# Optimization experiments

Measured on AMD Instinct MI355X. Metric: run time of the kernel, lower is better.

## Reference

```python
import jax, jax.numpy as jnp
import numpy as np

N_NODES = 131072
N_EDGES = 1048576
N_FEAT = 8
H = 128
H6 = 256
N_PROB = 64


def _gru_cell(m, h, Wih, Whh, bih, bhh):
    # PyTorch GRUCell semantics
    gi = m @ Wih.T + bih  # [N, 3H]
    gh = h @ Whh.T + bhh
    i_r, i_z, i_n = jnp.split(gi, 3, axis=-1)
    h_r, h_z, h_n = jnp.split(gh, 3, axis=-1)
    r = jax.nn.sigmoid(i_r + h_r)
    z = jax.nn.sigmoid(i_z + h_z)
    n = jnp.tanh(i_n + r * h_n)
    return (1.0 - z) * n + z * h


def _gated_graph_conv(x, src, dst, ew, W, Wih, Whh, bih, bhh):
    # PyG GatedGraphConv(out_channels=H, num_layers=2); in_channels == out_channels so no padding
    h = x
    for l in range(2):
        t = h @ W[l]                      # node-level transform [N, H]
        msg = t[src] * ew[:, None]        # gather + edge scaling [E, H]
        agg = jax.ops.segment_sum(msg, dst, num_segments=x.shape[0])  # scatter-add
        h = _gru_cell(agg, h, Wih, Whh, bih, bhh)
    return h


def _forward(G, edge_index, edge_weight, edge_attribute, segment_ids,
             W_emb1, b_emb1, W_emb2, b_emb2,
             conv1_W, conv1_Wih, conv1_Whh, conv1_bih, conv1_bhh,
             conv2_W, conv2_Wih, conv2_Whh, conv2_bih, conv2_bhh,
             W_g1, b_g1, W_g2, b_g2, W_l, b_l, W_l2, b_l2, W_l3, b_l3):
    src, dst = edge_index[0], edge_index[1]
    x = jax.nn.relu(G @ W_emb1 + b_emb1)
    x = jax.nn.relu(x @ W_emb2 + b_emb2)
    x = jax.nn.relu(_gated_graph_conv(x, src, dst, edge_weight, conv1_W, conv1_Wih, conv1_Whh, conv1_bih, conv1_bhh))
    x = jax.nn.relu(_gated_graph_conv(x, src, dst, edge_weight, conv2_W, conv2_Wih, conv2_Whh, conv2_bih, conv2_bhh))
    x = jax.nn.relu(x @ W_g1 + b_g1)
    x = x @ W_g2 + b_g2                   # node embeddings [N, H]
    # per-problem segment mean (replaces the python loop over contiguous slices)
    sums = jax.ops.segment_sum(x, segment_ids, num_segments=N_PROB)
    counts = jax.ops.segment_sum(jnp.ones((x.shape[0], 1), x.dtype), segment_ids, num_segments=N_PROB)
    gmean = sums / jnp.maximum(counts, 1.0)
    u = jnp.concatenate([x, gmean[segment_ids]], axis=-1)  # [N, 2H]
    u = jax.nn.relu(u @ W_l + b_l)
    u = jax.nn.relu(u @ W_l2 + b_l2)
    u = u @ W_l3 + b_l3                   # [N, 1]
    return u


def setup_inputs() -> dict:
    key = jax.random.key(0)
    ks = jax.random.split(key, 40)
    s = 0.05
    rn = lambda k, shp: (jax.random.normal(k, shp, jnp.float32) * s)
    inp = {}
    inp["G"] = jax.random.normal(ks[0], (N_NODES, N_FEAT), jnp.float32)
    inp["edge_index"] = jax.random.randint(ks[1], (2, N_EDGES), 0, N_NODES, jnp.int32)
    inp["edge_weight"] = jax.random.uniform(ks[2], (N_EDGES,), jnp.float32)
    inp["edge_attribute"] = jax.random.normal(ks[3], (N_EDGES,), jnp.float32)
    inp["segment_ids"] = jnp.sort(jax.random.randint(ks[4], (N_NODES,), 0, N_PROB, jnp.int32))
    inp["W_emb1"] = rn(ks[5], (N_FEAT, H)); inp["b_emb1"] = jnp.zeros((H,), jnp.float32)
    inp["W_emb2"] = rn(ks[6], (H, H));      inp["b_emb2"] = jnp.zeros((H,), jnp.float32)
    inp["conv1_W"] = rn(ks[7], (2, H, H))
    inp["conv1_Wih"] = rn(ks[8], (3 * H, H)); inp["conv1_Whh"] = rn(ks[9], (3 * H, H))
    inp["conv1_bih"] = jnp.zeros((3 * H,), jnp.float32); inp["conv1_bhh"] = jnp.zeros((3 * H,), jnp.float32)
    inp["conv2_W"] = rn(ks[10], (2, H, H))
    inp["conv2_Wih"] = rn(ks[11], (3 * H, H)); inp["conv2_Whh"] = rn(ks[12], (3 * H, H))
    inp["conv2_bih"] = jnp.zeros((3 * H,), jnp.float32); inp["conv2_bhh"] = jnp.zeros((3 * H,), jnp.float32)
    inp["W_g1"] = rn(ks[13], (H, H)); inp["b_g1"] = jnp.zeros((H,), jnp.float32)
    inp["W_g2"] = rn(ks[14], (H, H)); inp["b_g2"] = jnp.zeros((H,), jnp.float32)
    inp["W_l"] = rn(ks[15], (2 * H, H6)); inp["b_l"] = jnp.zeros((H6,), jnp.float32)
    inp["W_l2"] = rn(ks[16], (H6, H)); inp["b_l2"] = jnp.zeros((H,), jnp.float32)
    inp["W_l3"] = rn(ks[17], (H, 1)); inp["b_l3"] = jnp.zeros((1,), jnp.float32)
    return inp


def reference(G, edge_index, edge_weight, edge_attribute, segment_ids,
              W_emb1, b_emb1, W_emb2, b_emb2,
              conv1_W, conv1_Wih, conv1_Whh, conv1_bih, conv1_bhh,
              conv2_W, conv2_Wih, conv2_Whh, conv2_bih, conv2_bhh,
              W_g1, b_g1, W_g2, b_g2, W_l, b_l, W_l2, b_l2, W_l3, b_l3):
    return _forward(G, edge_index, edge_weight, edge_attribute, segment_ids,
                    W_emb1, b_emb1, W_emb2, b_emb2,
                    conv1_W, conv1_Wih, conv1_Whh, conv1_bih, conv1_bhh,
                    conv2_W, conv2_Wih, conv2_Whh, conv2_bih, conv2_bhh,
                    W_g1, b_g1, W_g2, b_g2, W_l, b_l, W_l2, b_l2, W_l3, b_l3)
```

## Files before the change

kernel.cpp:

```cpp
#include <hip/hip_runtime.h>
#include <cstdint>
#include <cstddef>

#define NNODES 131072
#define NEDGES 1048576
#define NPROB  64

typedef _Float16 half8 __attribute__((ext_vector_type(8)));
typedef _Float16 half4v __attribute__((ext_vector_type(4)));
typedef _Float16 half2v __attribute__((ext_vector_type(2)));
typedef float float4v __attribute__((ext_vector_type(4)));

__device__ __forceinline__ float fsigm(float x) {
    return __builtin_amdgcn_rcpf(1.0f + __expf(-x));
}
__device__ __forceinline__ float ftanh(float x) {
    return 1.0f - 2.0f * __builtin_amdgcn_rcpf(__expf(2.0f * x) + 1.0f);
}

__device__ __forceinline__ void async16(void* lds, const void* g) {
    __builtin_amdgcn_global_load_lds(
        (const __attribute__((address_space(1))) uint32_t*)g,
        (__attribute__((address_space(3))) uint32_t*)lds, 16, 0, 0);
}

__global__ __launch_bounds__(256) void cvt16(const float* __restrict__ s,
                                             _Float16* __restrict__ d, int n)
{
    int i = blockIdx.x * 256 + threadIdx.x;
    if (i < n) d[i] = (_Float16)s[i];
}

__global__ __launch_bounds__(256) void tr_cvt(const float* __restrict__ src,
    _Float16* __restrict__ dst, int K, int M, int sstride)
{
    int i = blockIdx.x * 256 + threadIdx.x;
    if (i < M * K) {
        int m = i / K, k = i % K;
        dst[i] = (_Float16)src[(size_t)k * sstride + m];
    }
}

__global__ __launch_bounds__(256) void deg_hist(const int* __restrict__ dst,
                                                int* __restrict__ deg)
{
    int e = blockIdx.x * 256 + threadIdx.x;
    atomicAdd(&deg[dst[e]], 1);
}

__global__ __launch_bounds__(256) void scan1(const int* __restrict__ deg,
    int* __restrict__ offs, int* __restrict__ bsum)
{
    __shared__ int s[256];
    int b = blockIdx.x, tid = threadIdx.x;
    int4 v = ((const int4*)deg)[b * 256 + tid];
    int t0 = v.x, t1 = t0 + v.y, t2 = t1 + v.z, t3 = t2 + v.w;
    s[tid] = t3;
    __syncthreads();
    for (int off = 1; off < 256; off <<= 1) {
        int x = (tid >= off) ? s[tid - off] : 0;
        __syncthreads();
        if (tid >= off) s[tid] += x;
        __syncthreads();
    }
    int excl = tid ? s[tid - 1] : 0;
    int4 o; o.x = excl; o.y = excl + t0; o.z = excl + t1; o.w = excl + t2;
    ((int4*)offs)[b * 256 + tid] = o;
    if (tid == 255) bsum[b] = s[255];
}

__global__ __launch_bounds__(128) void scan2(int* __restrict__ bsum)
{
    __shared__ int s[128];
    int tid = threadIdx.x;
    s[tid] = bsum[tid];
    __syncthreads();
    for (int off = 1; off < 128; off <<= 1) {
        int x = (tid >= off) ? s[tid - off] : 0;
        __syncthreads();
        if (tid >= off) s[tid] += x;
        __syncthreads();
    }
    bsum[tid] = tid ? s[tid - 1] : 0;
}

__global__ __launch_bounds__(256) void scan3(int* __restrict__ offs,
    const int* __restrict__ bsum, int* __restrict__ pos)
{
    int i = blockIdx.x * 256 + threadIdx.x;
    int v = offs[i] + bsum[i >> 10];
    offs[i] = v;
    pos[i] = v;
    if (i == 0) offs[NNODES] = NEDGES;
}

__global__ __launch_bounds__(256) void csr_fill(const int* __restrict__ src,
    const int* __restrict__ dst, const float* __restrict__ ew,
    int* __restrict__ pos, int2* __restrict__ csr)
{
    int e = blockIdx.x * 256 + threadIdx.x;
    int slot = atomicAdd(&pos[dst[e]], 1);
    csr[slot] = make_int2(src[e], __float_as_int(ew[e]));
}

__global__ __launch_bounds__(256) void gather_agg(const _Float16* __restrict__ t,
    const int2* __restrict__ csr, const int* __restrict__ offs,
    _Float16* __restrict__ agg)
{
    int node = blockIdx.x * 4 + (threadIdx.x >> 6);
    int lane = threadIdx.x & 63;
    int i = offs[node], end = offs[node + 1];
    float a0 = 0.0f, a1 = 0.0f;
    int2 p;
    if (i < end) p = csr[i];
    while (i < end) {
        int2 cur = p;
        if (i + 1 < end) p = csr[i + 1];
        float w = __int_as_float(cur.y);
        half2v v = *(const half2v*)(t + (size_t)cur.x * 128 + lane * 2);
        a0 = fmaf((float)v[0], w, a0);
        a1 = fmaf((float)v[1], w, a1);
        ++i;
    }
    half2v o; o[0] = (_Float16)a0; o[1] = (_Float16)a1;
    *(half2v*)(agg + (size_t)node * 128 + lane * 2) = o;
}

__global__ __launch_bounds__(256) void emb1_kernel(const float* __restrict__ G,
    const float* __restrict__ W1, const float* __restrict__ b1, _Float16* __restrict__ Y)
{
    int idx = blockIdx.x * 256 + threadIdx.x;
    int n = idx >> 7, c = idx & 127;
    const float* g = G + (size_t)n * 8;
    float y = b1[c];
#pragma unroll
    for (int k = 0; k < 8; ++k) y = fmaf(g[k], W1[k * 128 + c], y);
    Y[(size_t)n * 128 + c] = (_Float16)fmaxf(y, 0.0f);
}

template<int K, int MCH, bool INF16, bool RELU, bool SEGADD>
__global__ __launch_bounds__(256, 2) void gemm_mfma(
    const void* __restrict__ Xin, int xstride,
    const _Float16* __restrict__ Wt,
    const float* __restrict__ bias,
    _Float16* __restrict__ out1, int ostride,
    const float* __restrict__ gproj, const int* __restrict__ seg)
{
    constexpr int ROWB = 2 * K;
    constexpr int SPR  = K / 8;
    __shared__ __align__(16) char Xs[128 * ROWB];
    __shared__ __align__(16) char Ws[128 * ROWB];
    const int tid = threadIdx.x, wid = tid >> 6, l = tid & 63;
    const int lr = l & 15, lk = l >> 4;
    const int wrow = wid * 32;

    for (int mc = 0; mc < MCH; ++mc) {
        __syncthreads();
        {
            const _Float16* wsrc = Wt + (size_t)mc * 128 * K;
            for (int s0 = wid * 64; s0 < 128 * SPR; s0 += 256) {
                int s = s0 + l;
                int row = s / SPR, sub = s % SPR;
                int ksub = sub ^ (row & 7);
                async16(Ws + s0 * 16, (const char*)(wsrc + (size_t)row * K) + ksub * 16);
            }
        }
        asm volatile("s_waitcnt vmcnt(0)" ::: "memory");
        __syncthreads();

        half8 bfr[32];
        if constexpr (K == 128) {
#pragma unroll
            for (int ct = 0; ct < 8; ++ct)
#pragma unroll
                for (int ks = 0; ks < 4; ++ks) {
                    int row = ct * 16 + lr;
                    bfr[ct * 4 + ks] = *(const half8*)(Ws + row * ROWB +
                        ((ks * 64 + lk * 16) ^ ((row & 7) << 4)));
                }
        }

        for (int t = blockIdx.x; t < NNODES / 128; t += gridDim.x) {
            const int nbase = t * 128;
            __syncthreads();
            if constexpr (INF16) {
                const _Float16* xsrc = (const _Float16*)Xin;
                for (int s0 = wid * 64; s0 < 128 * SPR; s0 += 256) {
                    int s = s0 + l;
                    int row = s / SPR, sub = s % SPR;
                    int ksub = sub ^ (row & 7);
                    async16(Xs + s0 * 16,
                            (const char*)(xsrc + (size_t)(nbase + row) * xstride) + ksub * 16);
                }
                asm volatile("s_waitcnt vmcnt(0)" ::: "memory");
            } else {
                const float* xsrc = (const float*)Xin;
                for (int s = tid; s < 128 * SPR; s += 256) {
                    int row = s / SPR, sub = s % SPR;
                    int ksub = sub ^ (row & 7);
                    const float* p = xsrc + (size_t)(nbase + row) * xstride + ksub * 8;
                    float4 u = ((const float4*)p)[0];
                    float4 v = ((const float4*)p)[1];
                    half8 hv;
                    hv[0] = (_Float16)u.x; hv[1] = (_Float16)u.y;
                    hv[2] = (_Float16)u.z; hv[3] = (_Float16)u.w;
                    hv[4] = (_Float16)v.x; hv[5] = (_Float16)v.y;
                    hv[6] = (_Float16)v.z; hv[7] = (_Float16)v.w;
                    *(half8*)(Xs + s * 16) = hv;
                }
            }
            __syncthreads();

            float4v acc[2][8];
#pragma unroll
            for (int i = 0; i < 2; ++i)
#pragma unroll
                for (int j = 0; j < 8; ++j)
#pragma unroll
                    for (int q = 0; q < 4; ++q) acc[i][j][q] = 0.0f;

            if constexpr (K == 128) {
#pragma unroll
                for (int rt = 0; rt < 2; ++rt) {
                    half8 a[4];
                    int row = wrow + rt * 16 + lr;
#pragma unroll
                    for (int ks = 0; ks < 4; ++ks)
                        a[ks] = *(const half8*)(Xs + row * ROWB +
                            ((ks * 64 + lk * 16) ^ ((row & 7) << 4)));
#pragma unroll
                    for (int ct = 0; ct < 8; ++ct)
#pragma unroll
                        for (int ks = 0; ks < 4; ++ks)
                            acc[rt][ct] = __builtin_amdgcn_mfma_f32_16x16x32_f16(
                                a[ks], bfr[ct * 4 + ks], acc[rt][ct], 0, 0, 0);
                }
            } else {
#pragma unroll
                for (int kc = 0; kc < 2; ++kc) {
#pragma unroll
                    for (int ct = 0; ct < 8; ++ct)
#pragma unroll
                        for (int ks = 0; ks < 4; ++ks) {
                            int row = ct * 16 + lr;
                            bfr[ct * 4 + ks] = *(const half8*)(Ws + row * ROWB +
                                (((kc * 4 + ks) * 64 + lk * 16) ^ ((row & 7) << 4)));
                        }
#pragma unroll
                    for (int rt = 0; rt < 2; ++rt) {
                        half8 a[4];
                        int row = wrow + rt * 16 + lr;
#pragma unroll
                        for (int ks = 0; ks < 4; ++ks)
                            a[ks] = *(const half8*)(Xs + row * ROWB +
                                (((kc * 4 + ks) * 64 + lk * 16) ^ ((row & 7) << 4)));
#pragma unroll
                        for (int ct = 0; ct < 8; ++ct)
#pragma unroll
                            for (int ks = 0; ks < 4; ++ks)
                                acc[rt][ct] = __builtin_amdgcn_mfma_f32_16x16x32_f16(
                                    a[ks], bfr[ct * 4 + ks], acc[rt][ct], 0, 0, 0);
                    }
                }
            }

#pragma unroll
            for (int rt = 0; rt < 2; ++rt)
#pragma unroll
            for (int ct = 0; ct < 8; ++ct) {
                const int col = ct * 16 + lr;
                float bv = 0.0f;
                if (bias) bv = bias[mc * 128 + col];
#pragma unroll
                for (int j = 0; j < 4; ++j) {
                    const int n = nbase + wrow + rt * 16 + lk * 4 + j;
                    float v = acc[rt][ct][j] + bv;
                    if constexpr (SEGADD)
                        v += gproj[(size_t)seg[n] * 256 + mc * 128 + col];
                    if constexpr (RELU) v = fmaxf(v, 0.0f);
                    out1[(size_t)n * ostride + mc * 128 + col] = (_Float16)v;
                }
            }
        }
    }
}

__global__ __launch_bounds__(512, 2) void gru_fused(
    const _Float16* __restrict__ agg,
    _Float16* h,
    const _Float16* __restrict__ Wih,
    const _Float16* __restrict__ Whh,
    const float* __restrict__ bih, const float* __restrict__ bhh,
    int relu_out)
{
    __shared__ __align__(16) char As[128 * 256];
    __shared__ __align__(16) char Hs[128 * 256];
    __shared__ __align__(16) char Wb[2][128 * 256];
    const int tid = threadIdx.x, wid = tid >> 6, l = tid & 63;
    const int lr = l & 15, lk = l >> 4;
    const int wr = wid >> 1, wc = wid & 1;
    const int nbase = blockIdx.x * 128;

    auto stageT = [&](char* dst, const _Float16* src) {
        for (int s0 = wid * 64; s0 < 2048; s0 += 512) {
            int s = s0 + l;
            int row = s >> 4, sub = s & 15;
            int ksub = sub ^ (row & 7);
            async16(dst + s0 * 16, (const char*)(src + (size_t)row * 128) + ksub * 16);
        }
    };

    stageT(As, agg + (size_t)nbase * 128);
    stageT(Hs, h + (size_t)nbase * 128);
    stageT(Wb[0], Wih);

    float4v accA[2][4], accB[2][4], rg[2][4], zg[2][4];
    half8 aAg[2][4], aH[2][4];

#pragma unroll
    for (int c = 0; c < 6; ++c) {
        asm volatile("s_waitcnt vmcnt(0)" ::: "memory");
        __syncthreads();
        if (c < 5) {
            const int nc = c + 1;
            const _Float16* wsrc = ((nc & 1) ? Whh : Wih) + (size_t)(nc >> 1) * 16384;
            stageT(Wb[nc & 1], wsrc);
        }
        if (c == 0) {
#pragma unroll
            for (int rt = 0; rt < 2; ++rt) {
                const int row = wr * 32 + rt * 16 + lr;
#pragma unroll
                for (int ks = 0; ks < 4; ++ks) {
                    const int off = row * 256 + ((ks * 64 + lk * 16) ^ ((row & 7) << 4));
                    aAg[rt][ks] = *(const half8*)(As + off);
                    aH[rt][ks]  = *(const half8*)(Hs + off);
                }
            }
        }

        auto& af  = (c & 1) ? aH : aAg;
        auto& acc = (c & 1) ? accB : accA;
#pragma unroll
        for (int rt = 0; rt < 2; ++rt)
#pragma unroll
            for (int ct = 0; ct < 4; ++ct)
#pragma unroll
                for (int q = 0; q < 4; ++q) acc[rt][ct][q] = 0.0f;

        const char* wb = Wb[c & 1];
#pragma unroll
        for (int ct = 0; ct < 4; ++ct) {
            const int rowb = wc * 64 + ct * 16 + lr;
#pragma unroll
            for (int ks = 0; ks < 4; ++ks) {
                half8 b = *(const half8*)(wb + rowb * 256 +
                    ((ks * 64 + lk * 16) ^ ((rowb & 7) << 4)));
                acc[0][ct] = __builtin_amdgcn_mfma_f32_16x16x32_f16(af[0][ks], b, acc[0][ct], 0, 0, 0);
                acc[1][ct] = __builtin_amdgcn_mfma_f32_16x16x32_f16(af[1][ks], b, acc[1][ct], 0, 0, 0);
            }
        }

        if (c == 1) {
#pragma unroll
            for (int rt = 0; rt < 2; ++rt)
#pragma unroll
            for (int ct = 0; ct < 4; ++ct) {
                const int col = wc * 64 + ct * 16 + lr;
                const float bb = bih[col] + bhh[col];
#pragma unroll
                for (int j = 0; j < 4; ++j)
                    rg[rt][ct][j] = fsigm(accA[rt][ct][j] + accB[rt][ct][j] + bb);
            }
        } else if (c == 3) {
#pragma unroll
            for (int rt = 0; rt < 2; ++rt)
#pragma unroll
            for (int ct = 0; ct < 4; ++ct) {
                const int col = wc * 64 + ct * 16 + lr;
                const float bb = bih[128 + col] + bhh[128 + col];
#pragma unroll
                for (int j = 0; j < 4; ++j)
                    zg[rt][ct][j] = fsigm(accA[rt][ct][j] + accB[rt][ct][j] + bb);
            }
        } else if (c == 5) {
#pragma unroll
            for (int rt = 0; rt < 2; ++rt)
#pragma unroll
            for (int ct = 0; ct < 4; ++ct) {
                const int col = wc * 64 + ct * 16 + lr;
                const float bi = bih[256 + col], bh = bhh[256 + col];
                const int c2 = col * 2;
#pragma unroll
                for (int j = 0; j < 4; ++j) {
                    const int row = wr * 32 + rt * 16 + lk * 4 + j;
                    const int n = nbase + row;
                    float nv = ftanh(accA[rt][ct][j] + bi +
                                     rg[rt][ct][j] * (accB[rt][ct][j] + bh));
                    float hold = (float)*(const _Float16*)(Hs + row * 256 +
                        (((c2 >> 4) ^ (row & 7)) << 4) + (c2 & 15));
                    float z = zg[rt][ct][j];
                    float hn = (1.0f - z) * nv + z * hold;
                    if (relu_out) hn = fmaxf(hn, 0.0f);
                    h[(size_t)n * 128 + col] = (_Float16)hn;
                }
            }
        }
    }
}

__global__ __launch_bounds__(256) void seg_sum(const _Float16* __restrict__ x,
    const int* __restrict__ seg, float* __restrict__ sums, float* __restrict__ counts)
{
    int cg = threadIdx.x & 31, rs = threadIdx.x >> 5;
    int r0 = blockIdx.x * 256 + rs * 32;
    float a0 = 0, a1 = 0, a2 = 0, a3 = 0, cnt = 0;
    int cur = seg[r0];
    for (int i = 0; i < 32; ++i) {
        int n = r0 + i;
        int p = seg[n];
        if (p != cur) {
            atomicAdd(&sums[(size_t)cur * 128 + cg * 4 + 0], a0);
            atomicAdd(&sums[(size_t)cur * 128 + cg * 4 + 1], a1);
            atomicAdd(&sums[(size_t)cur * 128 + cg * 4 + 2], a2);
            atomicAdd(&sums[(size_t)cur * 128 + cg * 4 + 3], a3);
            if (cg == 0) atomicAdd(&counts[cur], cnt);
            a0 = a1 = a2 = a3 = 0; cnt = 0; cur = p;
        }
        half4v v = *(const half4v*)(x + (size_t)n * 128 + cg * 4);
        a0 += (float)v[0]; a1 += (float)v[1]; a2 += (float)v[2]; a3 += (float)v[3];
        cnt += 1.0f;
    }
    atomicAdd(&sums[(size_t)cur * 128 + cg * 4 + 0], a0);
    atomicAdd(&sums[(size_t)cur * 128 + cg * 4 + 1], a1);
    atomicAdd(&sums[(size_t)cur * 128 + cg * 4 + 2], a2);
    atomicAdd(&sums[(size_t)cur * 128 + cg * 4 + 3], a3);
    if (cg == 0) atomicAdd(&counts[cur], cnt);
}

__global__ __launch_bounds__(256) void gproj_kernel(const float* __restrict__ sums,
    const float* __restrict__ counts, const float* __restrict__ Wl,
    const float* __restrict__ bl, float* __restrict__ gproj)
{
    __shared__ float gm[128];
    int p = blockIdx.x, m = threadIdx.x;
    if (m < 128) gm[m] = sums[(size_t)p * 128 + m] / fmaxf(counts[p], 1.0f);
    __syncthreads();
    float acc = bl[m];
#pragma unroll 8
    for (int k = 0; k < 128; ++k)
        acc = fmaf(gm[k], Wl[(size_t)(128 + k) * 256 + m], acc);
    gproj[(size_t)p * 256 + m] = acc;
}

__global__ __launch_bounds__(256) void final_dot(const _Float16* __restrict__ u2,
    const float* __restrict__ wl3, const float* __restrict__ bl3, float* __restrict__ out)
{
    int gid = blockIdx.x * 256 + threadIdx.x;
    int n = gid >> 6, lane = gid & 63;
    half2v v = *(const half2v*)(u2 + (size_t)n * 128 + lane * 2);
    float s = (float)v[0] * wl3[lane * 2] + (float)v[1] * wl3[lane * 2 + 1];
#pragma unroll
    for (int off = 32; off; off >>= 1) s += __shfl_xor(s, off);
    if (lane == 0) out[n] = s + bl3[0];
}

extern "C" void kernel_launch(void* const* d_in, const int* in_sizes, int n_in,
                              void* d_out, int out_size, void* d_ws, size_t ws_size,
                              hipStream_t stream)
{
    (void)in_sizes; (void)n_in; (void)out_size; (void)ws_size;

    const float* G     = (const float*)d_in[0];
    const int*   ei    = (const int*)d_in[1];
    const float* ew    = (const float*)d_in[2];
    const int*   seg   = (const int*)d_in[4];
    const float* Wemb1 = (const float*)d_in[5];  const float* bemb1 = (const float*)d_in[6];
    const float* Wemb2 = (const float*)d_in[7];  const float* bemb2 = (const float*)d_in[8];
    const float* c1W   = (const float*)d_in[9];
    const float* c1Wih = (const float*)d_in[10]; const float* c1Whh = (const float*)d_in[11];
    const float* c1bih = (const float*)d_in[12]; const float* c1bhh = (const float*)d_in[13];
    const float* c2W   = (const float*)d_in[14];
    const float* c2Wih = (const float*)d_in[15]; const float* c2Whh = (const float*)d_in[16];
    const float* c2bih = (const float*)d_in[17]; const float* c2bhh = (const float*)d_in[18];
    const float* Wg1   = (const float*)d_in[19]; const float* bg1   = (const float*)d_in[20];
    const float* Wg2   = (const float*)d_in[21]; const float* bg2   = (const float*)d_in[22];
    const float* Wl    = (const float*)d_in[23]; const float* bl    = (const float*)d_in[24];
    const float* Wl2   = (const float*)d_in[25]; const float* bl2   = (const float*)d_in[26];
    const float* Wl3   = (const float*)d_in[27]; const float* bl3   = (const float*)d_in[28];

    const int* srcp = ei;
    const int* dstp = ei + NEDGES;

    char* ws = (char*)d_ws;
    const size_t NBH  = (size_t)NNODES * 128 * 2;
    const size_t G3B  = (size_t)NNODES * 384 * 2;

    _Float16* hA   = (_Float16*)ws;
    _Float16* hB   = (_Float16*)(ws + NBH);
    _Float16* g    = (_Float16*)(ws + 2 * NBH);
    _Float16* aggH = (_Float16*)(ws + 2 * NBH + G3B);
    char*     aux  = ws + 3 * NBH + G3B;
    float* sums   = (float*)aux;
    float* counts = (float*)(aux + 32768);
    float* gproj  = (float*)(aux + 33792);
    int*  deg   = (int*)(aux + 33792 + 65536);
    int*  offs  = deg + NNODES;
    int*  pos   = offs + NNODES + 64;
    int2* csr   = (int2*)(pos + NNODES);
    _Float16* wt = (_Float16*)((char*)csr + (size_t)NEDGES * 8);

    _Float16* wt_emb2 = wt;
    _Float16* wt_c1a  = wt + 16384;
    _Float16* wt_c1b  = wt + 2 * 16384;
    _Float16* wt_c2a  = wt + 3 * 16384;
    _Float16* wt_c2b  = wt + 4 * 16384;
    _Float16* wt_g1   = wt + 5 * 16384;
    _Float16* wt_g2   = wt + 6 * 16384;
    _Float16* wt_l    = wt + 7 * 16384;
    _Float16* wt_l2   = wt + 7 * 16384 + 32768;
    _Float16* wt_ih1  = wt + 7 * 16384 + 2 * 32768;
    _Float16* wt_hh1  = wt_ih1 + 49152;
    _Float16* wt_ih2  = wt_ih1 + 2 * 49152;
    _Float16* wt_hh2  = wt_ih1 + 3 * 49152;

    tr_cvt<<<64, 256, 0, stream>>>(Wemb2, wt_emb2, 128, 128, 128);
    tr_cvt<<<64, 256, 0, stream>>>(c1W,           wt_c1a, 128, 128, 128);
    tr_cvt<<<64, 256, 0, stream>>>(c1W + 16384,   wt_c1b, 128, 128, 128);
    tr_cvt<<<64, 256, 0, stream>>>(c2W,           wt_c2a, 128, 128, 128);
    tr_cvt<<<64, 256, 0, stream>>>(c2W + 16384,   wt_c2b, 128, 128, 128);
    tr_cvt<<<64, 256, 0, stream>>>(Wg1, wt_g1, 128, 128, 128);
    tr_cvt<<<64, 256, 0, stream>>>(Wg2, wt_g2, 128, 128, 128);
    tr_cvt<<<128, 256, 0, stream>>>(Wl,  wt_l,  128, 256, 256);
    tr_cvt<<<128, 256, 0, stream>>>(Wl2, wt_l2, 256, 128, 128);
    cvt16<<<192, 256, 0, stream>>>(c1Wih, wt_ih1, 49152);
    cvt16<<<192, 256, 0, stream>>>(c1Whh, wt_hh1, 49152);
    cvt16<<<192, 256, 0, stream>>>(c2Wih, wt_ih2, 49152);
    cvt16<<<192, 256, 0, stream>>>(c2Whh, wt_hh2, 49152);

    hipMemsetAsync(deg, 0, NNODES * 4, stream);
    deg_hist<<<NEDGES / 256, 256, 0, stream>>>(dstp, deg);
    scan1<<<128, 256, 0, stream>>>(deg, offs, pos);
    scan2<<<1, 128, 0, stream>>>(pos);
    scan3<<<NNODES / 256, 256, 0, stream>>>(offs, pos, deg);
    csr_fill<<<NEDGES / 256, 256, 0, stream>>>(srcp, dstp, ew, deg, csr);

    emb1_kernel<<<NNODES * 128 / 256, 256, 0, stream>>>(G, Wemb1, bemb1, hB);
    gemm_mfma<128, 1, true, true, false><<<512, 256, 0, stream>>>(
        hB, 128, wt_emb2, bemb2, hA, 128, nullptr, nullptr);

    const _Float16* convW[2][2] = { { wt_c1a, wt_c1b }, { wt_c2a, wt_c2b } };
    const _Float16* wih[2] = { wt_ih1, wt_ih2 };
    const _Float16* whh[2] = { wt_hh1, wt_hh2 };
    const float* bihs[2] = { c1bih, c2bih };
    const float* bhhs[2] = { c1bhh, c2bhh };
    for (int cv = 0; cv < 2; ++cv) {
        for (int lyr = 0; lyr < 2; ++lyr) {
            gemm_mfma<128, 1, true, false, false><<<512, 256, 0, stream>>>(
                hA, 128, convW[cv][lyr], nullptr, hB, 128, nullptr, nullptr);
            gather_agg<<<NNODES / 4, 256, 0, stream>>>(hB, csr, offs, aggH);
            gru_fused<<<NNODES / 128, 512, 0, stream>>>(
                aggH, hA, wih[cv], whh[cv], bihs[cv], bhhs[cv], (lyr == 1) ? 1 : 0);
        }
    }

    gemm_mfma<128, 1, true, true, false><<<512, 256, 0, stream>>>(
        hA, 128, wt_g1, bg1, hB, 128, nullptr, nullptr);
    gemm_mfma<128, 1, true, false, false><<<512, 256, 0, stream>>>(
        hB, 128, wt_g2, bg2, hA, 128, nullptr, nullptr);

    hipMemsetAsync(sums, 0, 33792, stream);
    seg_sum<<<NNODES / 256, 256, 0, stream>>>(hA, seg, sums, counts);
    gproj_kernel<<<NPROB, 256, 0, stream>>>(sums, counts, Wl, bl, gproj);

    gemm_mfma<128, 2, true, true, true><<<512, 256, 0, stream>>>(
        hA, 128, wt_l, nullptr, g, 256, gproj, seg);
    gemm_mfma<256, 1, true, true, false><<<256, 256, 0, stream>>>(
        g, 256, wt_l2, bl2, hB, 128, nullptr, nullptr);
    final_dot<<<NNODES * 64 / 256, 256, 0, stream>>>(hB, Wl3, bl3, (float*)d_out);
}
```

Baseline: 1.102 ms.

## Fold conv and head weights into combined matrices, unroll gather loop

Since segment_sum is linear, the per-layer node transform W is folded into the GRU input weights (Wih·Wᵀ), which removes four full-size GEMMs and a write/read of t per layer. Gathering now runs directly on h. Wg2 is likewise folded into the head's Wl, with the gmean projection and bias precomputed, which drops another full GEMM. The gather loop is unrolled by four to keep more independent loads in flight. The trade-off is extra small weight-combination kernels and fp16 rounding of the combined weights.

```diff
diff --git a/kernel.cpp b/kernel.cpp
--- a/kernel.cpp
+++ b/kernel.cpp
@@ -39,6 +39,54 @@
         int m = i / K, k = i % K;
         dst[i] = (_Float16)src[(size_t)k * sstride + m];
     }
+}
+
+__global__ __launch_bounds__(256) void combine_gru(const float* __restrict__ Wih,
+    const float* __restrict__ W, _Float16* __restrict__ outw)
+{
+    int i = blockIdx.x * 256 + threadIdx.x;
+    int g = i >> 7, j = i & 127;
+    const float* a = Wih + (size_t)g * 128;
+    const float* b = W + (size_t)j * 128;
+    float s = 0.0f;
+#pragma unroll 8
+    for (int k = 0; k < 128; ++k) s = fmaf(a[k], b[k], s);
+    outw[i] = (_Float16)s;
+}
+
+__global__ __launch_bounds__(256) void combine_headA(const float* __restrict__ Wg2,
+    const float* __restrict__ Wl, _Float16* __restrict__ At)
+{
+    int i = blockIdx.x * 256 + threadIdx.x;
+    int m = i >> 7, j = i & 127;
+    float s = 0.0f;
+#pragma unroll 8
+    for (int k = 0; k < 128; ++k)
+        s = fmaf(Wg2[(size_t)j * 128 + k], Wl[(size_t)k * 256 + m], s);
+    At[i] = (_Float16)s;
+}
+
+__global__ __launch_bounds__(256) void combine_headB(const float* __restrict__ Wg2,
+    const float* __restrict__ Wl, float* __restrict__ Bf)
+{
+    int i = blockIdx.x * 256 + threadIdx.x;
+    int t = i >> 8, m = i & 255;
+    float s = 0.0f;
+#pragma unroll 8
+    for (int k = 0; k < 128; ++k)
+        s = fmaf(Wg2[(size_t)t * 128 + k], Wl[(size_t)(128 + k) * 256 + m], s);
+    Bf[i] = s;
+}
+
+__global__ __launch_bounds__(256) void combine_c(const float* __restrict__ bg2,
+    const float* __restrict__ Wl, const float* __restrict__ bl, float* __restrict__ cvec)
+{
+    int m = threadIdx.x;
+    float s = bl[m];
+#pragma unroll 8
+    for (int k = 0; k < 128; ++k)
+        s = fmaf(bg2[k], Wl[(size_t)k * 256 + m] + Wl[(size_t)(128 + k) * 256 + m], s);
+    cvec[m] = s;
 }
 
 __global__ __launch_bounds__(256) void deg_hist(const int* __restrict__ dst,
@@ -111,16 +159,25 @@
     int lane = threadIdx.x & 63;
     int i = offs[node], end = offs[node + 1];
     float a0 = 0.0f, a1 = 0.0f;
-    int2 p;
-    if (i < end) p = csr[i];
-    while (i < end) {
-        int2 cur = p;
-        if (i + 1 < end) p = csr[i + 1];
-        float w = __int_as_float(cur.y);
-        half2v v = *(const half2v*)(t + (size_t)cur.x * 128 + lane * 2);
+    for (; i + 4 <= end; i += 4) {
+        int2 e0 = csr[i], e1 = csr[i + 1], e2 = csr[i + 2], e3 = csr[i + 3];
+        half2v v0 = *(const half2v*)(t + (size_t)e0.x * 128 + lane * 2);
+        half2v v1 = *(const half2v*)(t + (size_t)e1.x * 128 + lane * 2);
+        half2v v2 = *(const half2v*)(t + (size_t)e2.x * 128 + lane * 2);
+        half2v v3 = *(const half2v*)(t + (size_t)e3.x * 128 + lane * 2);
+        float w0 = __int_as_float(e0.y), w1 = __int_as_float(e1.y);
+        float w2 = __int_as_float(e2.y), w3 = __int_as_float(e3.y);
+        a0 = fmaf((float)v0[0], w0, a0); a1 = fmaf((float)v0[1], w0, a1);
+        a0 = fmaf((float)v1[0], w1, a0); a1 = fmaf((float)v1[1], w1, a1);
+        a0 = fmaf((float)v2[0], w2, a0); a1 = fmaf((float)v2[1], w2, a1);
+        a0 = fmaf((float)v3[0], w3, a0); a1 = fmaf((float)v3[1], w3, a1);
+    }
+    for (; i < end; ++i) {
+        int2 e = csr[i];
+        float w = __int_as_float(e.y);
+        half2v v = *(const half2v*)(t + (size_t)e.x * 128 + lane * 2);
         a0 = fmaf((float)v[0], w, a0);
         a1 = fmaf((float)v[1], w, a1);
-        ++i;
     }
     half2v o; o[0] = (_Float16)a0; o[1] = (_Float16)a1;
     *(half2v*)(agg + (size_t)node * 128 + lane * 2) = o;
@@ -438,19 +495,19 @@
     if (cg == 0) atomicAdd(&counts[cur], cnt);
 }
 
-__global__ __launch_bounds__(256) void gproj_kernel(const float* __restrict__ sums,
-    const float* __restrict__ counts, const float* __restrict__ Wl,
-    const float* __restrict__ bl, float* __restrict__ gproj)
+__global__ __launch_bounds__(256) void gproj2_kernel(const float* __restrict__ sums,
+    const float* __restrict__ counts, const float* __restrict__ Bf,
+    const float* __restrict__ cvec, float* __restrict__ gproj2)
 {
     __shared__ float gm[128];
     int p = blockIdx.x, m = threadIdx.x;
     if (m < 128) gm[m] = sums[(size_t)p * 128 + m] / fmaxf(counts[p], 1.0f);
     __syncthreads();
-    float acc = bl[m];
+    float acc = cvec[m];
 #pragma unroll 8
     for (int k = 0; k < 128; ++k)
-        acc = fmaf(gm[k], Wl[(size_t)(128 + k) * 256 + m], acc);
-    gproj[(size_t)p * 256 + m] = acc;
+        acc = fmaf(gm[k], Bf[(size_t)k * 256 + m], acc);
+    gproj2[(size_t)p * 256 + m] = acc;
 }
 
 __global__ __launch_bounds__(256) void final_dot(const _Float16* __restrict__ u2,
@@ -493,50 +550,48 @@
     const int* dstp = ei + NEDGES;
 
     char* ws = (char*)d_ws;
-    const size_t NBH  = (size_t)NNODES * 128 * 2;
-    const size_t G3B  = (size_t)NNODES * 384 * 2;
+    const size_t NBH = (size_t)NNODES * 128 * 2;
+    const size_t U1B = (size_t)NNODES * 256 * 2;
 
     _Float16* hA   = (_Float16*)ws;
     _Float16* hB   = (_Float16*)(ws + NBH);
-    _Float16* g    = (_Float16*)(ws + 2 * NBH);
-    _Float16* aggH = (_Float16*)(ws + 2 * NBH + G3B);
-    char*     aux  = ws + 3 * NBH + G3B;
-    float* sums   = (float*)aux;
-    float* counts = (float*)(aux + 32768);
-    float* gproj  = (float*)(aux + 33792);
-    int*  deg   = (int*)(aux + 33792 + 65536);
-    int*  offs  = deg + NNODES;
-    int*  pos   = offs + NNODES + 64;
-    int2* csr   = (int2*)(pos + NNODES);
-    _Float16* wt = (_Float16*)((char*)csr + (size_t)NEDGES * 8);
-
-    _Float16* wt_emb2 = wt;
-    _Float16* wt_c1a  = wt + 16384;
-    _Float16* wt_c1b  = wt + 2 * 16384;
-    _Float16* wt_c2a  = wt + 3 * 16384;
-    _Float16* wt_c2b  = wt + 4 * 16384;
-    _Float16* wt_g1   = wt + 5 * 16384;
-    _Float16* wt_g2   = wt + 6 * 16384;
-    _Float16* wt_l    = wt + 7 * 16384;
-    _Float16* wt_l2   = wt + 7 * 16384 + 32768;
-    _Float16* wt_ih1  = wt + 7 * 16384 + 2 * 32768;
-    _Float16* wt_hh1  = wt_ih1 + 49152;
-    _Float16* wt_ih2  = wt_ih1 + 2 * 49152;
-    _Float16* wt_hh2  = wt_ih1 + 3 * 49152;
+    _Float16* u1   = (_Float16*)(ws + 2 * NBH);
+    _Float16* aggH = (_Float16*)(ws + 2 * NBH + U1B);
+    char*     aux  = ws + 3 * NBH + U1B;
+    float* sums    = (float*)aux;
+    float* counts  = (float*)(aux + 32768);
+    float* gproj2  = (float*)(aux + 33792);
+    int*   deg     = (int*)(aux + 33792 + 65536);
+    int*   offs    = deg + NNODES;
+    int*   pos     = offs + NNODES + 64;
+    int2*  csr     = (int2*)(pos + NNODES);
+    char*  wtb     = (char*)csr + (size_t)NEDGES * 8;
+
+    _Float16* wt_emb2 = (_Float16*)wtb;
+    _Float16* wt_g1   = wt_emb2 + 16384;
+    _Float16* wt_l2   = wt_g1 + 16384;
+    _Float16* wt_hh1  = wt_l2 + 32768;
+    _Float16* wt_hh2  = wt_hh1 + 49152;
+    _Float16* wc00    = wt_hh2 + 49152;
+    _Float16* wc01    = wc00 + 49152;
+    _Float16* wc10    = wc01 + 49152;
+    _Float16* wc11    = wc10 + 49152;
+    _Float16* At      = wc11 + 49152;
+    float*    Bf      = (float*)(At + 32768);
+    float*    cvec    = Bf + 32768;
 
     tr_cvt<<<64, 256, 0, stream>>>(Wemb2, wt_emb2, 128, 128, 128);
-    tr_cvt<<<64, 256, 0, stream>>>(c1W,           wt_c1a, 128, 128, 128);
-    tr_cvt<<<64, 256, 0, stream>>>(c1W + 16384,   wt_c1b, 128, 128, 128);
-    tr_cvt<<<64, 256, 0, stream>>>(c2W,           wt_c2a, 128, 128, 128);
-    tr_cvt<<<64, 256, 0, stream>>>(c2W + 16384,   wt_c2b, 128, 128, 128);
     tr_cvt<<<64, 256, 0, stream>>>(Wg1, wt_g1, 128, 128, 128);
-    tr_cvt<<<64, 256, 0, stream>>>(Wg2, wt_g2, 128, 128, 128);
-    tr_cvt<<<128, 256, 0, stream>>>(Wl,  wt_l,  128, 256, 256);
     tr_cvt<<<128, 256, 0, stream>>>(Wl2, wt_l2, 256, 128, 128);
-    cvt16<<<192, 256, 0, stream>>>(c1Wih, wt_ih1, 49152);
     cvt16<<<192, 256, 0, stream>>>(c1Whh, wt_hh1, 49152);
-    cvt16<<<192, 256, 0, stream>>>(c2Wih, wt_ih2, 49152);
     cvt16<<<192, 256, 0, stream>>>(c2Whh, wt_hh2, 49152);
+    combine_gru<<<192, 256, 0, stream>>>(c1Wih, c1W,         wc00);
+    combine_gru<<<192, 256, 0, stream>>>(c1Wih, c1W + 16384, wc01);
+    combine_gru<<<192, 256, 0, stream>>>(c2Wih, c2W,         wc10);
+    combine_gru<<<192, 256, 0, stream>>>(c2Wih, c2W + 16384, wc11);
+    combine_headA<<<128, 256, 0, stream>>>(Wg2, Wl, At);
+    combine_headB<<<128, 256, 0, stream>>>(Wg2, Wl, Bf);
+    combine_c<<<1, 256, 0, stream>>>(bg2, Wl, bl, cvec);
 
     hipMemsetAsync(deg, 0, NNODES * 4, stream);
     deg_hist<<<NEDGES / 256, 256, 0, stream>>>(dstp, deg);
@@ -549,33 +604,28 @@
     gemm_mfma<128, 1, true, true, false><<<512, 256, 0, stream>>>(
         hB, 128, wt_emb2, bemb2, hA, 128, nullptr, nullptr);
 
-    const _Float16* convW[2][2] = { { wt_c1a, wt_c1b }, { wt_c2a, wt_c2b } };
-    const _Float16* wih[2] = { wt_ih1, wt_ih2 };
+    const _Float16* wcs[2][2] = { { wc00, wc01 }, { wc10, wc11 } };
     const _Float16* whh[2] = { wt_hh1, wt_hh2 };
     const float* bihs[2] = { c1bih, c2bih };
     const float* bhhs[2] = { c1bhh, c2bhh };
     for (int cv = 0; cv < 2; ++cv) {
         for (int lyr = 0; lyr < 2; ++lyr) {
-            gemm_mfma<128, 1, true, false, false><<<512, 256, 0, stream>>>(
-                hA, 128, convW[cv][lyr], nullptr, hB, 128, nullptr, nullptr);
-            gather_agg<<<NNODES / 4, 256, 0, stream>>>(hB, csr, offs, aggH);
+            gather_agg<<<NNODES / 4, 256, 0, stream>>>(hA, csr, offs, aggH);
             gru_fused<<<NNODES / 128, 512, 0, stream>>>(
-                aggH, hA, wih[cv], whh[cv], bihs[cv], bhhs[cv], (lyr == 1) ? 1 : 0);
+                aggH, hA, wcs[cv][lyr], whh[cv], bihs[cv], bhhs[cv], (lyr == 1) ? 1 : 0);
         }
     }
 
     gemm_mfma<128, 1, true, true, false><<<512, 256, 0, stream>>>(
         hA, 128, wt_g1, bg1, hB, 128, nullptr, nullptr);
-    gemm_mfma<128, 1, true, false, false><<<512, 256, 0, stream>>>(
-        hB, 128, wt_g2, bg2, hA, 128, nullptr, nullptr);
 
     hipMemsetAsync(sums, 0, 33792, stream);
-    seg_sum<<<NNODES / 256, 256, 0, stream>>>(hA, seg, sums, counts);
-    gproj_kernel<<<NPROB, 256, 0, stream>>>(sums, counts, Wl, bl, gproj);
+    seg_sum<<<NNODES / 256, 256, 0, stream>>>(hB, seg, sums, counts);
+    gproj2_kernel<<<NPROB, 256, 0, stream>>>(sums, counts, Bf, cvec, gproj2);
 
     gemm_mfma<128, 2, true, true, true><<<512, 256, 0, stream>>>(
-        hA, 128, wt_l, nullptr, g, 256, gproj, seg);
+        hB, 128, At, nullptr, u1, 256, gproj2, seg);
     gemm_mfma<256, 1, true, true, false><<<256, 256, 0, stream>>>(
-        g, 256, wt_l2, bl2, hB, 128, nullptr, nullptr);
-    final_dot<<<NNODES * 64 / 256, 256, 0, stream>>>(hB, Wl3, bl3, (float*)d_out);
-}
+        u1, 256, wt_l2, bl2, hA, 128, nullptr, nullptr);
+    final_dot<<<NNODES * 64 / 256, 256, 0, stream>>>(hA, Wl3, bl3, (float*)d_out);
+}
```

New measurement: 968.7 us. 12.1% less time.
